# Optimization experiments

Hardware: AMD Instinct MI355X
Metric: run time of the kernel (lower is better)

## Reference

```python
import jax, jax.numpy as jnp
import numpy as np

LN_EPS = 1e-6


def setup_inputs() -> dict:
    key = jax.random.key(0)
    ks = jax.random.split(key, 8)
    B, T, V, r, c, D = 1, 2048, 50257, 16, 16, 1024
    rc = r * c
    return {
        "input_ids": jax.random.randint(ks[0], (B, T), 0, V),
        "token_to_mu_w": jax.random.normal(ks[1], (rc, V), jnp.float32) * 0.02,  # nn.Linear(V, rc).weight
        "pos_embedding": jax.random.normal(ks[2], (1, T, r, c), jnp.float32) * 0.02,
        "w1": jax.random.normal(ks[3], (D, rc), jnp.float32) * 0.05,  # Linear(rc, D).weight
        "b1": jnp.zeros((D,), jnp.float32),
        "ln_w": jnp.ones((D,), jnp.float32),
        "ln_b": jnp.zeros((D,), jnp.float32),
        "w2": jax.random.normal(ks[4], (V, D), jnp.float32) * 0.02,  # Linear(D, V).weight
        "b2": jnp.zeros((V,), jnp.float32),
    }


def reference(input_ids, token_to_mu_w, pos_embedding, w1, b1, ln_w, ln_b, w2, b2):
    B, T = input_ids.shape
    r, c = pos_embedding.shape[2], pos_embedding.shape[3]
    # one_hot(input_ids) @ W^T is exactly a row-gather of W^T (single nonzero per row)
    MU = jnp.take(token_to_mu_w.T, input_ids, axis=0)          # [B, T, rc]
    MU = MU.reshape(B, T, r, c) + pos_embedding[:, :T]         # [B, T, r, c]
    # n_layers = 0: no transformer blocks; dropout is identity in eval
    x = MU.reshape(B, T, r * c)
    h = jax.nn.gelu(jnp.einsum('btk,dk->btd', x, w1) + b1, approximate=False)
    mean = jnp.mean(h, axis=-1, keepdims=True)
    var = jnp.mean(jnp.square(h - mean), axis=-1, keepdims=True)
    h = (h - mean) * jax.lax.rsqrt(var + LN_EPS) * ln_w + ln_b
    logits = jnp.einsum('btd,vd->btv', h, w2) + b2             # [B, T, V]
    return logits, MU
```

## Files before the change

### kernel.cpp

```cpp
#include <hip/hip_runtime.h>
#include <hip/hip_bf16.h>
#include <math.h>

#define T_LEN 2048
#define RC 256
#define DIM 1024
#define VOCAB 50257
#define NT 32
#define SLOT 8192

using short8  = __attribute__((ext_vector_type(8))) short;
using f32x4   = __attribute__((ext_vector_type(4))) float;

#define VMCNT(n) asm volatile("s_waitcnt vmcnt(" #n ")" ::: "memory")
#define LGKM(n)  asm volatile("s_waitcnt lgkmcnt(" #n ")" ::: "memory")
#define SCHED_FENCE() __builtin_amdgcn_sched_barrier(0)

__device__ __forceinline__ unsigned short f2bf(float f) {
    unsigned int u = __float_as_uint(f);
    u += 0x7fffu + ((u >> 16) & 1u);
    return (unsigned short)(u >> 16);
}

__device__ __forceinline__ unsigned int cvt_pk_bf16(float a, float b) {
    unsigned int r;
    asm volatile("v_cvt_pk_bf16_f32 %0, %1, %2" : "=v"(r) : "v"(a), "v"(b));
    return r;
}

__device__ __forceinline__ void async_load16(void* lds, const void* g) {
    __builtin_amdgcn_global_load_lds(
        (const __attribute__((address_space(1))) void*)g,
        (__attribute__((address_space(3))) void*)lds,
        16, 0, 0);
}

__global__ __launch_bounds__(256) void mu_kernel(
    const int* __restrict__ ids, const float* __restrict__ tokw,
    const float* __restrict__ pos, float* __restrict__ mu) {
    int t = blockIdx.x, k = threadIdx.x;
    int id = ids[t];
    float v = tokw[(size_t)k * VOCAB + id] + pos[t * RC + k];
    mu[t * RC + k] = v;
}

__global__ __launch_bounds__(256) void gemm1_gelu_kernel(
    const float* __restrict__ mu, const float* __restrict__ w1,
    const float* __restrict__ b1, float* __restrict__ hpre) {
    __shared__ float xs[16][RC];
    const int tg = blockIdx.x, ng = blockIdx.y, tid = threadIdx.x;
    const int t0 = tg * 16;
    {
        const float4* src = (const float4*)(mu + (size_t)t0 * RC);
        float4* dst = (float4*)&xs[0][0];
        #pragma unroll
        for (int i = 0; i < 4; ++i) dst[tid + 256 * i] = src[tid + 256 * i];
    }
    __syncthreads();
    const int d = ng * 256 + tid;
    float acc[16];
    const float bias = b1[d];
    #pragma unroll
    for (int t = 0; t < 16; ++t) acc[t] = bias;
    const float4* w1r = (const float4*)(w1 + (size_t)d * RC);
    for (int k4 = 0; k4 < RC / 4; ++k4) {
        const float4 w = w1r[k4];
        #pragma unroll
        for (int t = 0; t < 16; ++t) {
            const float4 xv = *(const float4*)&xs[t][k4 * 4];
            acc[t] += w.x * xv.x + w.y * xv.y + w.z * xv.z + w.w * xv.w;
        }
    }
    #pragma unroll
    for (int t = 0; t < 16; ++t) {
        float x = acc[t];
        float g = 0.5f * x * (1.0f + erff(x * 0.70710678118654752f));
        hpre[(size_t)(t0 + t) * DIM + d] = g;
    }
}

__global__ __launch_bounds__(256) void ln_kernel(
    const float* __restrict__ hpre, const float* __restrict__ lnw,
    const float* __restrict__ lnb, unsigned short* __restrict__ h) {
    const int t = blockIdx.x, tid = threadIdx.x;
    const float4 v = ((const float4*)(hpre + (size_t)t * DIM))[tid];
    float s  = v.x + v.y + v.z + v.w;
    float ss = v.x * v.x + v.y * v.y + v.z * v.z + v.w * v.w;
    #pragma unroll
    for (int off = 32; off > 0; off >>= 1) {
        s  += __shfl_down(s, off, 64);
        ss += __shfl_down(ss, off, 64);
    }
    __shared__ float red[8];
    const int wid = tid >> 6, lane = tid & 63;
    if (lane == 0) { red[wid] = s; red[4 + wid] = ss; }
    __syncthreads();
    const float S  = red[0] + red[1] + red[2] + red[3];
    const float SS = red[4] + red[5] + red[6] + red[7];
    const float mean = S * (1.0f / DIM);
    const float var  = SS * (1.0f / DIM) - mean * mean;
    const float inv  = 1.0f / sqrtf(var + 1e-6f);
    const float4 wv = ((const float4*)lnw)[tid];
    const float4 bv = ((const float4*)lnb)[tid];
    ushort4 o;
    o.x = f2bf((v.x - mean) * inv * wv.x + bv.x);
    o.y = f2bf((v.y - mean) * inv * wv.y + bv.y);
    o.z = f2bf((v.z - mean) * inv * wv.z + bv.z);
    o.w = f2bf((v.w - mean) * inv * wv.w + bv.w);
    ((ushort4*)h)[(size_t)t * (DIM / 4) + tid] = o;
}

__global__ __launch_bounds__(256) void cvt_kernel(
    const float* __restrict__ src, unsigned int* __restrict__ dst, int n8) {
    int i = blockIdx.x * 256 + threadIdx.x;
    const int stride = gridDim.x * 256;
    for (; i < n8; i += stride) {
        const float4 a = ((const float4*)src)[2 * i];
        const float4 b = ((const float4*)src)[2 * i + 1];
        uint4 o;
        o.x = cvt_pk_bf16(a.x, a.y);
        o.y = cvt_pk_bf16(a.z, a.w);
        o.z = cvt_pk_bf16(b.x, b.y);
        o.w = cvt_pk_bf16(b.z, b.w);
        ((uint4*)dst)[i] = o;
    }
}

__device__ __forceinline__ void stage_A512(
    const unsigned short* __restrict__ A, unsigned short* dst,
    int m0, int kt, int tid, int gsrc) {
    #pragma unroll
    for (int p = 0; p < 2; ++p) {
        const int idx = p * 512 + tid;
        const int row = idx >> 2;
        async_load16(dst + (size_t)idx * 8,
                     A + (size_t)(m0 + row) * DIM + kt * 32 + gsrc * 8);
    }
}
__device__ __forceinline__ void stage_B512(
    const unsigned short* __restrict__ B, unsigned short* dst,
    int n0, int kt, int tid, int gsrc) {
    #pragma unroll
    for (int p = 0; p < 2; ++p) {
        const int idx = p * 512 + tid;
        int row = n0 + (idx >> 2); if (row > VOCAB - 1) row = VOCAB - 1;
        async_load16(dst + (size_t)idx * 8,
                     B + (size_t)row * DIM + kt * 32 + gsrc * 8);
    }
}

#define TILE_BODY(T, BF_USE, BF_LOAD)                                          \
  {                                                                            \
    const int t_  = (T);                                                       \
    const int cur = t_ & 3;                                                    \
    const int nxt = (t_ + 1) & 3;                                              \
    const int st  = (t_ + 3) & 3;                                              \
    const unsigned short* As_t = As + cur * SLOT;                              \
                       \
    _Pragma("unroll")                                                          \
    for (int m = 0; m < 4; ++m)                                                \
        af_o[m] = *(const short8*)(As_t + (arow0 + (m + 4) * 16) * 32 + xr);   \
    if (t_ + 3 < NT)                                                           \
        stage_A512(A, As + st * SLOT, m0, t_ + 3, tid, gsrc);                  \
    SCHED_FENCE();                                                             \
    LGKM(4);                           \
    SCHED_FENCE();                                                             \
    __builtin_amdgcn_s_setprio(1);                                             \
    _Pragma("unroll")                                                          \
    for (int m = 0; m < 4; ++m)                                                \
        _Pragma("unroll")                                                      \
        for (int n = 0; n < 4; ++n)                                            \
            acc[m][n] = __builtin_amdgcn_mfma_f32_16x16x32_bf16(               \
                af_e[m], BF_USE[n], acc[m][n], 0, 0, 0);                       \
    __builtin_amdgcn_s_setprio(0);                                             \
    SCHED_FENCE();                                                             \
    if (t_ + 3 < NT) { VMCNT(6); } else { VMCNT(0); }                          \
    __builtin_amdgcn_s_barrier();        \
                        \
    if (t_ + 1 < NT) {                                                         \
        const unsigned short* As_n = As + nxt * SLOT;                          \
        const unsigned short* Bs_n = Bs + nxt * SLOT;                          \
        _Pragma("unroll")                                                      \
        for (int m = 0; m < 4; ++m)                                            \
            af_e[m] = *(const short8*)(As_n + (arow0 + m * 16) * 32 + xr);     \
        _Pragma("unroll")                                                      \
        for (int n = 0; n < 4; ++n)                                            \
            BF_LOAD[n] = *(const short8*)(Bs_n + (brow0 + n * 16) * 32 + xr);  \
    }                                                                          \
    if (t_ + 3 < NT)                                                           \
        stage_B512(B, Bs + st * SLOT, n0, t_ + 3, tid, gsrc);                  \
    SCHED_FENCE();                                                             \
    if (t_ + 1 < NT) { LGKM(8); } else { LGKM(0); }           \
    SCHED_FENCE();                                                             \
    __builtin_amdgcn_s_setprio(1);                                             \
    _Pragma("unroll")                                                          \
    for (int m = 0; m < 4; ++m)                                                \
        _Pragma("unroll")                                                      \
        for (int n = 0; n < 4; ++n)                                            \
            acc[m + 4][n] = __builtin_amdgcn_mfma_f32_16x16x32_bf16(           \
                af_o[m], BF_USE[n], acc[m + 4][n], 0, 0, 0);                   \
    __builtin_amdgcn_s_setprio(0);                                             \
    SCHED_FENCE();                                                             \
    __builtin_amdgcn_s_barrier();     \
  }

__global__ __launch_bounds__(512, 2) void gemm2_kernel(
    const unsigned short* __restrict__ A, const unsigned short* __restrict__ B,
    const float* __restrict__ b2, float* __restrict__ out) {
    __shared__ unsigned short As[4 * SLOT];
    __shared__ unsigned short Bs[4 * SLOT];

    const int tid  = threadIdx.x;
    const int cpx  = gridDim.x >> 3;
    const int wgid = (blockIdx.x & 7) * cpx + (blockIdx.x >> 3);
    const int m0   = (wgid & 7) << 8;
    const int n0   = (wgid >> 3) << 8;

    const int lane = tid & 63;
    const int lr   = lane & 15;
    const int lk   = lane >> 4;
    const int wid  = tid >> 6;
    const int wr   = wid >> 2;
    const int wc   = wid & 3;
    const int xr   = (lk ^ ((lr >> 1) & 3)) * 8;
    const int arow0 = wr * 128 + lr;
    const int brow0 = wc * 64 + lr;
    const int gsrc = (tid & 3) ^ ((tid >> 3) & 3);

    f32x4 acc[8][4];
    #pragma unroll
    for (int m = 0; m < 8; ++m)
        #pragma unroll
        for (int n = 0; n < 4; ++n) acc[m][n] = {0.f, 0.f, 0.f, 0.f};

    stage_A512(A, As, m0, 0, tid, gsrc);
    stage_B512(B, Bs, n0, 0, tid, gsrc);
    SCHED_FENCE();
    stage_A512(A, As + SLOT, m0, 1, tid, gsrc);
    stage_B512(B, Bs + SLOT, n0, 1, tid, gsrc);
    SCHED_FENCE();
    stage_A512(A, As + 2 * SLOT, m0, 2, tid, gsrc);
    stage_B512(B, Bs + 2 * SLOT, n0, 2, tid, gsrc);
    SCHED_FENCE();
    VMCNT(8);
    __builtin_amdgcn_s_barrier();

    short8 af_e[4], af_o[4], bfA[4], bfB[4];
    #pragma unroll
    for (int m = 0; m < 4; ++m)
        af_e[m] = *(const short8*)(As + (arow0 + m * 16) * 32 + xr);
    #pragma unroll
    for (int n = 0; n < 4; ++n)
        bfA[n] = *(const short8*)(Bs + (brow0 + n * 16) * 32 + xr);

    #pragma unroll 1
    for (int tt = 0; tt < NT; tt += 2) {
        TILE_BODY(tt,     bfA, bfB);
        TILE_BODY(tt + 1, bfB, bfA);
    }

    float bias[4]; int col[4]; bool ok[4];
    #pragma unroll
    for (int n = 0; n < 4; ++n) {
        col[n] = n0 + wc * 64 + n * 16 + lr;
        ok[n]  = col[n] < VOCAB;
        bias[n] = ok[n] ? b2[col[n]] : 0.f;
    }
    #pragma unroll
    for (int m = 0; m < 8; ++m) {
        const int row = m0 + wr * 128 + m * 16 + lk * 4;
        #pragma unroll
        for (int n = 0; n < 4; ++n) {
            if (ok[n]) {
                #pragma unroll
                for (int j = 0; j < 4; ++j)
                    out[(size_t)(row + j) * VOCAB + col[n]] = acc[m][n][j] + bias[n];
            }
        }
    }
}

extern "C" void kernel_launch(void* const* d_in, const int* in_sizes, int n_in,
                              void* d_out, int out_size, void* d_ws, size_t ws_size,
                              hipStream_t stream) {
    (void)in_sizes; (void)n_in; (void)out_size; (void)ws_size;
    const int*   ids  = (const int*)d_in[0];
    const float* tokw = (const float*)d_in[1];
    const float* pos  = (const float*)d_in[2];
    const float* w1   = (const float*)d_in[3];
    const float* b1   = (const float*)d_in[4];
    const float* lnw  = (const float*)d_in[5];
    const float* lnb  = (const float*)d_in[6];
    const float* w2   = (const float*)d_in[7];
    const float* b2   = (const float*)d_in[8];

    float* logits = (float*)d_out;
    float* mu_out = logits + (size_t)T_LEN * VOCAB;

    unsigned short* w2b = (unsigned short*)d_ws;
    unsigned short* hb  = (unsigned short*)((char*)d_ws + (size_t)VOCAB * DIM * 2);
    float* hpre = logits;

    mu_kernel<<<dim3(T_LEN), dim3(256), 0, stream>>>(ids, tokw, pos, mu_out);
    gemm1_gelu_kernel<<<dim3(T_LEN / 16, DIM / 256), dim3(256), 0, stream>>>(
        mu_out, w1, b1, hpre);
    ln_kernel<<<dim3(T_LEN), dim3(256), 0, stream>>>(hpre, lnw, lnb, hb);
    cvt_kernel<<<dim3(2048), dim3(256), 0, stream>>>(
        w2, (unsigned int*)w2b, (int)((size_t)VOCAB * DIM / 8));
    const int ntiles_n = (VOCAB + 255) / 256;
    gemm2_kernel<<<dim3(8 * ntiles_n), dim3(512), 0, stream>>>(hb, w2b, b2, logits);
}
```

Baseline: 461.0 us.

## Shrink gemm2 tile to 256x128 with 256 threads and triple-buffered LDS

The logits GEMM block tile is reduced from 256x256 with 8 waves to 256x128 with 4 waves, and the LDS pipeline drops from 4 stages to 3 (prefetch distance 2). B staging is halved and wait counts are adjusted. The aim is lower LDS use per block and more blocks for better occupancy and tail balance. In exchange, each block reuses A across half as many columns, which raises global and L2 traffic for A, and the shallower prefetch may expose more load latency.

```diff
diff --git a/kernel.cpp b/kernel.cpp
--- a/kernel.cpp
+++ b/kernel.cpp
@@ -7,7 +7,8 @@
 #define DIM 1024
 #define VOCAB 50257
 #define NT 32
-#define SLOT 8192
+#define ASLOT 8192
+#define BSLOT 4096
 
 using short8  = __attribute__((ext_vector_type(8))) short;
 using f32x4   = __attribute__((ext_vector_type(4))) float;
@@ -126,23 +127,23 @@
     }
 }
 
-__device__ __forceinline__ void stage_A512(
+__device__ __forceinline__ void stage_A256(
     const unsigned short* __restrict__ A, unsigned short* dst,
     int m0, int kt, int tid, int gsrc) {
     #pragma unroll
-    for (int p = 0; p < 2; ++p) {
-        const int idx = p * 512 + tid;
+    for (int p = 0; p < 4; ++p) {
+        const int idx = p * 256 + tid;
         const int row = idx >> 2;
         async_load16(dst + (size_t)idx * 8,
                      A + (size_t)(m0 + row) * DIM + kt * 32 + gsrc * 8);
     }
 }
-__device__ __forceinline__ void stage_B512(
+__device__ __forceinline__ void stage_B256(
     const unsigned short* __restrict__ B, unsigned short* dst,
     int n0, int kt, int tid, int gsrc) {
     #pragma unroll
     for (int p = 0; p < 2; ++p) {
-        const int idx = p * 512 + tid;
+        const int idx = p * 256 + tid;
         int row = n0 + (idx >> 2); if (row > VOCAB - 1) row = VOCAB - 1;
         async_load16(dst + (size_t)idx * 8,
                      B + (size_t)row * DIM + kt * 32 + gsrc * 8);
@@ -152,16 +153,16 @@
 #define TILE_BODY(T, BF_USE, BF_LOAD)                                          \
   {                                                                            \
     const int t_  = (T);                                                       \
-    const int cur = t_ & 3;                                                    \
-    const int nxt = (t_ + 1) & 3;                                              \
-    const int st  = (t_ + 3) & 3;                                              \
-    const unsigned short* As_t = As + cur * SLOT;                              \
-                       \
+    const int cur = t_ % 3;                                                    \
+    const int nxt = (t_ + 1) % 3;                                              \
+    const int st  = (t_ + 2) % 3;                                              \
+    const unsigned short* As_t = As + cur * ASLOT;                             \
+                                 \
     _Pragma("unroll")                                                          \
     for (int m = 0; m < 4; ++m)                                                \
         af_o[m] = *(const short8*)(As_t + (arow0 + (m + 4) * 16) * 32 + xr);   \
-    if (t_ + 3 < NT)                                                           \
-        stage_A512(A, As + st * SLOT, m0, t_ + 3, tid, gsrc);                  \
+    if (t_ + 2 < NT)                                                           \
+        stage_A256(A, As + st * ASLOT, m0, t_ + 2, tid, gsrc);                 \
     SCHED_FENCE();                                                             \
     LGKM(4);                           \
     SCHED_FENCE();                                                             \
@@ -174,12 +175,12 @@
                 af_e[m], BF_USE[n], acc[m][n], 0, 0, 0);                       \
     __builtin_amdgcn_s_setprio(0);                                             \
     SCHED_FENCE();                                                             \
-    if (t_ + 3 < NT) { VMCNT(6); } else { VMCNT(0); }                          \
+    if (t_ < NT - 2) { VMCNT(4); } else { VMCNT(0); }                          \
     __builtin_amdgcn_s_barrier();        \
-                        \
+                                  \
     if (t_ + 1 < NT) {                                                         \
-        const unsigned short* As_n = As + nxt * SLOT;                          \
-        const unsigned short* Bs_n = Bs + nxt * SLOT;                          \
+        const unsigned short* As_n = As + nxt * ASLOT;                         \
+        const unsigned short* Bs_n = Bs + nxt * BSLOT;                         \
         _Pragma("unroll")                                                      \
         for (int m = 0; m < 4; ++m)                                            \
             af_e[m] = *(const short8*)(As_n + (arow0 + m * 16) * 32 + xr);     \
@@ -187,8 +188,8 @@
         for (int n = 0; n < 4; ++n)                                            \
             BF_LOAD[n] = *(const short8*)(Bs_n + (brow0 + n * 16) * 32 + xr);  \
     }                                                                          \
-    if (t_ + 3 < NT)                                                           \
-        stage_B512(B, Bs + st * SLOT, n0, t_ + 3, tid, gsrc);                  \
+    if (t_ + 2 < NT)                                                           \
+        stage_B256(B, Bs + st * BSLOT, n0, t_ + 2, tid, gsrc);                 \
     SCHED_FENCE();                                                             \
     if (t_ + 1 < NT) { LGKM(8); } else { LGKM(0); }           \
     SCHED_FENCE();                                                             \
@@ -204,24 +205,24 @@
     __builtin_amdgcn_s_barrier();     \
   }
 
-__global__ __launch_bounds__(512, 2) void gemm2_kernel(
+__global__ __launch_bounds__(256, 2) void gemm2_kernel(
     const unsigned short* __restrict__ A, const unsigned short* __restrict__ B,
     const float* __restrict__ b2, float* __restrict__ out) {
-    __shared__ unsigned short As[4 * SLOT];
-    __shared__ unsigned short Bs[4 * SLOT];
+    __shared__ unsigned short As[3 * ASLOT];
+    __shared__ unsigned short Bs[3 * BSLOT];
 
     const int tid  = threadIdx.x;
     const int cpx  = gridDim.x >> 3;
     const int wgid = (blockIdx.x & 7) * cpx + (blockIdx.x >> 3);
     const int m0   = (wgid & 7) << 8;
-    const int n0   = (wgid >> 3) << 8;
+    const int n0   = (wgid >> 3) << 7;
 
     const int lane = tid & 63;
     const int lr   = lane & 15;
     const int lk   = lane >> 4;
     const int wid  = tid >> 6;
-    const int wr   = wid >> 2;
-    const int wc   = wid & 3;
+    const int wr   = wid >> 1;
+    const int wc   = wid & 1;
     const int xr   = (lk ^ ((lr >> 1) & 3)) * 8;
     const int arow0 = wr * 128 + lr;
     const int brow0 = wc * 64 + lr;
@@ -233,16 +234,13 @@
         #pragma unroll
         for (int n = 0; n < 4; ++n) acc[m][n] = {0.f, 0.f, 0.f, 0.f};
 
-    stage_A512(A, As, m0, 0, tid, gsrc);
-    stage_B512(B, Bs, n0, 0, tid, gsrc);
+    stage_A256(A, As, m0, 0, tid, gsrc);
+    stage_B256(B, Bs, n0, 0, tid, gsrc);
     SCHED_FENCE();
-    stage_A512(A, As + SLOT, m0, 1, tid, gsrc);
-    stage_B512(B, Bs + SLOT, n0, 1, tid, gsrc);
+    stage_A256(A, As + ASLOT, m0, 1, tid, gsrc);
+    stage_B256(B, Bs + BSLOT, n0, 1, tid, gsrc);
     SCHED_FENCE();
-    stage_A512(A, As + 2 * SLOT, m0, 2, tid, gsrc);
-    stage_B512(B, Bs + 2 * SLOT, n0, 2, tid, gsrc);
-    SCHED_FENCE();
-    VMCNT(8);
+    VMCNT(6);
     __builtin_amdgcn_s_barrier();
 
     short8 af_e[4], af_o[4], bfA[4], bfB[4];
@@ -307,6 +305,6 @@
     ln_kernel<<<dim3(T_LEN), dim3(256), 0, stream>>>(hpre, lnw, lnb, hb);
     cvt_kernel<<<dim3(2048), dim3(256), 0, stream>>>(
         w2, (unsigned int*)w2b, (int)((size_t)VOCAB * DIM / 8));
-    const int ntiles_n = (VOCAB + 255) / 256;
-    gemm2_kernel<<<dim3(8 * ntiles_n), dim3(512), 0, stream>>>(hb, w2b, b2, logits);
-}
+    const int ntiles_n = (VOCAB + 127) / 128;
+    gemm2_kernel<<<dim3(8 * ntiles_n), dim3(256), 0, stream>>>(hb, w2b, b2, logits);
+}
```

After: 456.4 us. Within noise of the previous version (-1.0%).
